# Kernel optimization log

Hardware: AMD Instinct MI355X
Metric: run time of the kernel (lower is better)

Reference implementation:

```python
import jax, jax.numpy as jnp
import numpy as np

B, LQ, LK, D, DV = 8, 2048, 2048, 128, 128


def setup_inputs() -> dict:
    key = jax.random.key(0)
    ks = jax.random.split(key, 6)
    return {
        "query": jax.random.normal(ks[0], (B, LQ, D), dtype=jnp.float32),
        "key": jax.random.normal(ks[1], (B, LK, D), dtype=jnp.float32),
        "value": jax.random.normal(ks[2], (B, LK, DV), dtype=jnp.float32),
        "Wq": jax.random.normal(ks[3], (D, D), dtype=jnp.float32) * 0.08,
        "Wk": jax.random.normal(ks[4], (D, D), dtype=jnp.float32) * 0.08,
        "Wv": jax.random.normal(ks[5], (DV, DV), dtype=jnp.float32) * 0.08,
        "attention_mask": jnp.ones((B, 1, LK), dtype=jnp.int32),
    }


def reference(query, key, value, Wq, Wk, Wv, attention_mask):
    # Linear projections (right-multiplication, as in `x @ W`)
    q = query @ Wq          # [B, lq, n_ed]
    k = key @ Wk            # [B, lk, n_ed]
    v = value @ Wv          # [B, lk, n_ev]
    scale = 1.0 / np.sqrt(q.shape[-1])
    scores = jnp.einsum("bqd,bkd->bqk", q, k) * scale  # [B, lq, lk]
    # additive mask: 0 where attend, -inf where mask==0 (broadcasts)
    mask_vals = jnp.where(attention_mask == 0, -jnp.inf, 0.0).astype(scores.dtype)
    scores = scores + mask_vals
    attn = jax.nn.softmax(scores, axis=-1)
    return attn @ v         # [B, lq, n_ev]
```

## Files before the change

### kernel.cpp

```cpp
#include <hip/hip_runtime.h>
#include <hip/hip_bf16.h>

typedef unsigned short u16;
typedef unsigned int u32;
typedef __attribute__((ext_vector_type(8))) short s8v;
typedef __attribute__((ext_vector_type(4))) float f4v;
typedef __attribute__((ext_vector_type(16))) float f16v;

#define B_N 8
#define L_Q 2048
#define L_K 2048
#define DIM 128
#define KT  64
#define KSPLIT 4
#define KCHUNK (L_K / KSPLIT)

__device__ __forceinline__ u16 f2bf(float f) {
  union { float f; unsigned u; } v; v.f = f;
  return (u16)((v.u + 0x7fffu + ((v.u >> 16) & 1u)) >> 16);
}
__device__ __forceinline__ float bf2f(u16 u) {
  union { u32 u; float f; } v; v.u = ((u32)u) << 16; return v.f;
}
__device__ __forceinline__ u32 packbf2(float a, float b) {
  union { __hip_bfloat162 h; u32 u; } v;
  v.h = __float22bfloat162_rn(make_float2(a, b));
  return v.u;
}
__device__ __forceinline__ void async16(const u16* g, u16* l) {
  __builtin_amdgcn_global_load_lds(
      (const __attribute__((address_space(1))) u32*)(const void*)g,
      (__attribute__((address_space(3))) u32*)(void*)l, 16, 0, 0);
}


__global__ __launch_bounds__(256) void wprep(
    const float* __restrict__ Wq, const float* __restrict__ Wk,
    const float* __restrict__ Wv, u16* __restrict__ wbuf) {
  const int which = blockIdx.x;
  const int tid = threadIdx.x;
  const float* W = (which == 0) ? Wq : (which == 1) ? Wk : Wv;
  const float wscale = (which == 0) ? (1.44269504089f / 11.3137084990f) : 1.0f;
  u16* dst = wbuf + which * 16384;
#pragma unroll
  for (int i = 0; i < 16; ++i) {
    int f4i = tid + i * 256;
    float4 w4 = *(const float4*)(W + f4i * 4);
    int k = f4i >> 5, col = (f4i & 31) * 4;
    int ks = k >> 5, qd = (k & 31) >> 3, j = k & 7;
    float wv4[4] = {w4.x, w4.y, w4.z, w4.w};
#pragma unroll
    for (int c = 0; c < 4; ++c) {
      int n = col + c;
      dst[(ks * 8 + (n >> 4)) * 512 + (qd * 16 + (n & 15)) * 8 + j] = f2bf(wv4[c] * wscale);
    }
  }
}

__global__ __launch_bounds__(256) void proj_mfma(
    const float* __restrict__ query, const float* __restrict__ key,
    const float* __restrict__ value, const u16* __restrict__ wbuf,
    u16* __restrict__ qp, u16* __restrict__ kp, u16* __restrict__ vp) {
  __shared__ __align__(16) u16 Fb[8192];
  const int tid = threadIdx.x;
  const int bi = blockIdx.x;
  const int which = bi >> 8;
  const int sub = bi & 255;
  const int b = sub >> 5;
  const int rt = sub & 31;
  const float* X = (which == 0) ? query : (which == 1) ? key : value;
  const u16* Wfg = wbuf + which * 16384;

  const int w = tid >> 6, lane = tid & 63;
  const int ln = lane & 15, quad = lane >> 4;
  const int xrow = rt * 64 + w * 16 + ln;
  const float* Xr = X + ((size_t)b * L_Q + xrow) * DIM;

  s8v a[4];
#pragma unroll
  for (int ks = 0; ks < 4; ++ks) {
    float4 xa = *(const float4*)(Xr + ks * 32 + quad * 8);
    float4 xb = *(const float4*)(Xr + ks * 32 + quad * 8 + 4);
    s8v t;
    t[0] = (short)f2bf(xa.x); t[1] = (short)f2bf(xa.y);
    t[2] = (short)f2bf(xa.z); t[3] = (short)f2bf(xa.w);
    t[4] = (short)f2bf(xb.x); t[5] = (short)f2bf(xb.y);
    t[6] = (short)f2bf(xb.z); t[7] = (short)f2bf(xb.w);
    a[ks] = t;
  }

  f4v acc[8];
#pragma unroll
  for (int i = 0; i < 8; ++i) acc[i] = (f4v){0.f, 0.f, 0.f, 0.f};
#pragma unroll
  for (int ks = 0; ks < 4; ++ks)
#pragma unroll
    for (int nt = 0; nt < 8; ++nt) {
      s8v bw = *(const s8v*)(Wfg + (ks * 8 + nt) * 512 + lane * 8);
      acc[nt] = __builtin_amdgcn_mfma_f32_16x16x32_bf16(a[ks], bw, acc[nt], 0, 0, 0);
    }

  if (which < 2) {
#pragma unroll
    for (int nt = 0; nt < 8; ++nt) {
      int base = ((w >> 1) * 8 + nt) * 512 + ((ln >> 3) * 32 + (w & 1) * 16 + quad * 4) * 8 + (ln & 7);
#pragma unroll
      for (int r = 0; r < 4; ++r) Fb[base + r * 8] = f2bf(acc[nt][r]);
    }
  } else {
#pragma unroll
    for (int nt = 0; nt < 8; ++nt) {
      int base = (w * 4 + (nt >> 1)) * 512 + ((quad >> 1) * 32 + (nt & 1) * 16 + ln) * 8 + (quad & 1) * 4;
      *(u32*)&Fb[base]     = packbf2(acc[nt][0], acc[nt][1]);
      *(u32*)&Fb[base + 2] = packbf2(acc[nt][2], acc[nt][3]);
    }
  }
  __syncthreads();

  u16* Y = ((which == 0) ? qp : (which == 1) ? kp : vp) + (size_t)(b * 32 + rt) * 8192;
#pragma unroll
  for (int r = 0; r < 4; ++r) {
    int c = tid + r * 256;
    *(s8v*)(Y + c * 8) = *(const s8v*)(Fb + c * 8);
  }
}

__global__ __launch_bounds__(128, 2) void flash_split(
    const u16* __restrict__ qp, const u16* __restrict__ kp,
    const u16* __restrict__ vp, const int* __restrict__ mask,
    u16* __restrict__ po, float* __restrict__ ml) {
  __shared__ __align__(16) u16 Kf[8192];
  __shared__ __align__(16) u16 Vf[8192];
  __shared__ float alphaL[2][32];
  __shared__ float biasl[KT];

  const int tid = threadIdx.x;
  const int bi = blockIdx.x;
  const int b = bi & 7;
  const int rest = bi >> 3;
  const int p = rest & 3;
  const int qb = rest >> 2;
  const int w2 = tid >> 6;
  const int lane = tid & 63;
  const int qcol = lane & 31;
  const int H = lane >> 5;
  const bool Hb = (H != 0);

  const int* mb = mask + b * L_K;

  const u16* Qt = qp + (size_t)(b * 64 + qb * 2 + w2) * 4096;
  s8v aq[8];
#pragma unroll
  for (int c = 0; c < 8; ++c) aq[c] = *(const s8v*)(Qt + c * 512 + lane * 8);

  f16v o[4];
#pragma unroll
  for (int i = 0; i < 4; ++i)
#pragma unroll
    for (int r = 0; r < 16; ++r) o[i][r] = 0.f;
  float mrow = -__builtin_inff();
  float lrow = 0.f;

  for (int it = 0; it < KCHUNK / KT; ++it) {
    const int kt = p * (KCHUNK / KT) + it;
    const int k0 = kt * KT;
    const u16* Ktile = kp + (size_t)(b * 32 + kt) * 8192;
    const u16* Vtile = vp + (size_t)(b * 32 + kt) * 8192;
#pragma unroll
    for (int c8 = 0; c8 < 8; ++c8) {
      int f = w2 * 8 + c8;
      async16(Ktile + (size_t)(f * 64 + lane) * 8, Kf + f * 512);
      async16(Vtile + (size_t)(f * 64 + lane) * 8, Vf + f * 512);
    }
    int mv = mb[k0 + lane];
    bool allones = (__ballot(mv != 0) == ~0ull);
    if (!allones && tid < KT) biasl[tid] = (mv == 0) ? -__builtin_inff() : 0.f;
    __syncthreads();

    f16v s[2];
#pragma unroll
    for (int t = 0; t < 2; ++t)
#pragma unroll
      for (int r = 0; r < 16; ++r) s[t][r] = 0.f;
#pragma unroll
    for (int c = 0; c < 8; ++c) {
      s8v k0f = *(const s8v*)(Kf + c * 512 + lane * 8);
      s[0] = __builtin_amdgcn_mfma_f32_32x32x16_bf16(k0f, aq[c], s[0], 0, 0, 0);
      s8v k1f = *(const s8v*)(Kf + (8 + c) * 512 + lane * 8);
      s[1] = __builtin_amdgcn_mfma_f32_32x32x16_bf16(k1f, aq[c], s[1], 0, 0, 0);
    }
    if (!allones) {
#pragma unroll
      for (int t = 0; t < 2; ++t)
#pragma unroll
        for (int g = 0; g < 4; ++g) {
          float4 bt = *(const float4*)&biasl[t * 32 + g * 8 + 4 * H];
#pragma unroll
          for (int i = 0; i < 4; ++i) s[t][g * 4 + i] += bt.x * (i == 0) + bt.y * (i == 1) + bt.z * (i == 2) + bt.w * (i == 3);
        }
    }
    float m16 = s[0][0];
#pragma unroll
    for (int t = 0; t < 2; ++t)
#pragma unroll
      for (int r = 0; r < 16; ++r) m16 = fmaxf(m16, s[t][r]);
    m16 = fmaxf(m16, __shfl_xor(m16, 32, 64));

    float mn = fmaxf(mrow, m16);
    float alpha = __builtin_amdgcn_exp2f(fminf(mrow - mn, 0.f));
    mrow = mn;
    float rs = 0.f;
#pragma unroll
    for (int t = 0; t < 2; ++t)
#pragma unroll
      for (int r = 0; r < 16; ++r) {
        s[t][r] = __builtin_amdgcn_exp2f(fminf(s[t][r] - mn, 0.f));
        rs += s[t][r];
      }
    rs += __shfl_xor(rs, 32, 64);
    lrow = lrow * alpha + rs;

    if (H == 0) alphaL[w2][qcol] = alpha;

    u32 plo[2][4], phi[2][4];
#pragma unroll
    for (int t = 0; t < 2; ++t)
#pragma unroll
      for (int g = 0; g < 4; ++g) {
        plo[t][g] = packbf2(s[t][g * 4 + 0], s[t][g * 4 + 1]);
        phi[t][g] = packbf2(s[t][g * 4 + 2], s[t][g * 4 + 3]);
      }

#pragma unroll
    for (int g = 0; g < 4; ++g) {
      float4 av = *(const float4*)&alphaL[w2][g * 8 + 4 * H];
      float a4[4] = {av.x, av.y, av.z, av.w};
#pragma unroll
      for (int ntv = 0; ntv < 4; ++ntv)
#pragma unroll
        for (int i = 0; i < 4; ++i) o[ntv][g * 4 + i] *= a4[i];
    }

#pragma unroll
    for (int kc = 0; kc < 4; ++kc) {
      const int t = kc >> 1, gl = (kc & 1) * 2;
      u32 a_lo0 = plo[t][gl], a_hi0 = phi[t][gl];
      u32 a_lo1 = plo[t][gl + 1], a_hi1 = phi[t][gl + 1];
      u32 snd_lo = Hb ? a_lo0 : a_lo1;
      u32 snd_hi = Hb ? a_hi0 : a_hi1;
      u32 r_lo = (u32)__shfl_xor((int)snd_lo, 32, 64);
      u32 r_hi = (u32)__shfl_xor((int)snd_hi, 32, 64);
      union { u32 wd[4]; s8v v; } pa;
      pa.wd[0] = Hb ? r_lo : a_lo0;
      pa.wd[1] = Hb ? r_hi : a_hi0;
      pa.wd[2] = Hb ? a_lo1 : r_lo;
      pa.wd[3] = Hb ? a_hi1 : r_hi;
#pragma unroll
      for (int ntv = 0; ntv < 4; ++ntv) {
        s8v bv = *(const s8v*)(Vf + (kc * 4 + ntv) * 512 + lane * 8);
        o[ntv] = __builtin_amdgcn_mfma_f32_32x32x16_bf16(pa.v, bv, o[ntv], 0, 0, 0);
      }
    }
    __syncthreads();
  }

#pragma unroll
  for (int ntv = 0; ntv < 4; ++ntv)
#pragma unroll
    for (int reg = 0; reg < 16; ++reg) {
      int qloc = (reg & 3) + 8 * (reg >> 2) + 4 * H;
      size_t q = (size_t)b * L_Q + qb * 64 + w2 * 32 + qloc;
      po[(q * KSPLIT + p) * DIM + ntv * 32 + qcol] = f2bf(o[ntv][reg]);
    }
  if (H == 0) {
    size_t q = (size_t)b * L_Q + qb * 64 + w2 * 32 + qcol;
    *(float2*)&ml[(q * KSPLIT + p) * 2] = make_float2(mrow, lrow);
  }
}

__global__ __launch_bounds__(256) void combine(
    const u16* __restrict__ po, const float* __restrict__ ml,
    float* __restrict__ out) {
  const int t = threadIdx.x;
  const int lr = t >> 5, l32 = t & 31;
  const size_t q = (size_t)blockIdx.x * 8 + lr;

  float m[KSPLIT], l[KSPLIT];
#pragma unroll
  for (int p = 0; p < KSPLIT; ++p) {
    m[p] = ml[(q * KSPLIT + p) * 2 + 0];
    l[p] = ml[(q * KSPLIT + p) * 2 + 1];
  }
  float M = m[0];
#pragma unroll
  for (int p = 1; p < KSPLIT; ++p) M = fmaxf(M, m[p]);
  float wp[KSPLIT], L = 0.f;
#pragma unroll
  for (int p = 0; p < KSPLIT; ++p) {
    wp[p] = __builtin_amdgcn_exp2f(fminf(m[p] - M, 0.f));
    L += l[p] * wp[p];
  }
  float invL = 1.0f / L;

  float4 acc = make_float4(0.f, 0.f, 0.f, 0.f);
#pragma unroll
  for (int p = 0; p < KSPLIT; ++p) {
    ushort4 u = *(const ushort4*)(po + (q * KSPLIT + p) * DIM + l32 * 4);
    acc.x += wp[p] * bf2f(u.x); acc.y += wp[p] * bf2f(u.y);
    acc.z += wp[p] * bf2f(u.z); acc.w += wp[p] * bf2f(u.w);
  }
  acc.x *= invL; acc.y *= invL; acc.z *= invL; acc.w *= invL;
  *(float4*)(out + q * DIM + l32 * 4) = acc;
}

extern "C" void kernel_launch(void* const* d_in, const int* in_sizes, int n_in,
                              void* d_out, int out_size, void* d_ws, size_t ws_size,
                              hipStream_t stream) {
  const float* query = (const float*)d_in[0];
  const float* key   = (const float*)d_in[1];
  const float* value = (const float*)d_in[2];
  const float* Wq    = (const float*)d_in[3];
  const float* Wk    = (const float*)d_in[4];
  const float* Wv    = (const float*)d_in[5];
  const int*   mask  = (const int*)d_in[6];
  float* out = (float*)d_out;

  u16* qp = (u16*)d_ws;
  u16* kp = qp + (size_t)B_N * L_Q * DIM;
  u16* vp = kp + (size_t)B_N * L_K * DIM;
  u16* po = vp + (size_t)B_N * DIM * L_K;
  float* ml = (float*)(po + (size_t)B_N * L_Q * KSPLIT * DIM);
  u16* wbuf = (u16*)(ml + (size_t)B_N * L_Q * KSPLIT * 2);

  hipLaunchKernelGGL(wprep, dim3(3), dim3(256), 0, stream, Wq, Wk, Wv, wbuf);
  hipLaunchKernelGGL(proj_mfma, dim3(768), dim3(256), 0, stream,
                     query, key, value, wbuf, qp, kp, vp);
  hipLaunchKernelGGL(flash_split, dim3(1024), dim3(128), 0, stream,
                     qp, kp, vp, mask, po, ml);
  hipLaunchKernelGGL(combine, dim3((B_N * L_Q) / 8), dim3(256), 0, stream,
                     po, ml, out);
}
```

Measured before the change: 126.7 us.

## Double-buffer K/V tiles in flash kernel, widen blocks, stage weights in LDS

After: 122.6 us. 1.03x faster.

```diff
diff --git a/kernel.cpp b/kernel.cpp
--- a/kernel.cpp
+++ b/kernel.cpp
@@ -14,6 +14,7 @@
 #define KT  64
 #define KSPLIT 4
 #define KCHUNK (L_K / KSPLIT)
+#define NIT (KCHUNK / KT)
 
 __device__ __forceinline__ u16 f2bf(float f) {
   union { float f; unsigned u; } v; v.f = f;
@@ -57,10 +58,11 @@
   }
 }
 
-__global__ __launch_bounds__(256) void proj_mfma(
+__global__ __launch_bounds__(256, 3) void proj_mfma(
     const float* __restrict__ query, const float* __restrict__ key,
     const float* __restrict__ value, const u16* __restrict__ wbuf,
     u16* __restrict__ qp, u16* __restrict__ kp, u16* __restrict__ vp) {
+  __shared__ __align__(16) u16 Wf[16384];
   __shared__ __align__(16) u16 Fb[8192];
   const int tid = threadIdx.x;
   const int bi = blockIdx.x;
@@ -73,6 +75,13 @@
 
   const int w = tid >> 6, lane = tid & 63;
   const int ln = lane & 15, quad = lane >> 4;
+
+#pragma unroll
+  for (int c = 0; c < 8; ++c) {
+    int cg = w * 8 + c;
+    async16(Wfg + (size_t)(cg * 64 + lane) * 8, Wf + cg * 512);
+  }
+
   const int xrow = rt * 64 + w * 16 + ln;
   const float* Xr = X + ((size_t)b * L_Q + xrow) * DIM;
 
@@ -81,13 +90,14 @@
   for (int ks = 0; ks < 4; ++ks) {
     float4 xa = *(const float4*)(Xr + ks * 32 + quad * 8);
     float4 xb = *(const float4*)(Xr + ks * 32 + quad * 8 + 4);
-    s8v t;
-    t[0] = (short)f2bf(xa.x); t[1] = (short)f2bf(xa.y);
-    t[2] = (short)f2bf(xa.z); t[3] = (short)f2bf(xa.w);
-    t[4] = (short)f2bf(xb.x); t[5] = (short)f2bf(xb.y);
-    t[6] = (short)f2bf(xb.z); t[7] = (short)f2bf(xb.w);
-    a[ks] = t;
-  }
+    union { u32 wd[4]; s8v v; } t;
+    t.wd[0] = packbf2(xa.x, xa.y);
+    t.wd[1] = packbf2(xa.z, xa.w);
+    t.wd[2] = packbf2(xb.x, xb.y);
+    t.wd[3] = packbf2(xb.z, xb.w);
+    a[ks] = t.v;
+  }
+  __syncthreads();
 
   f4v acc[8];
 #pragma unroll
@@ -96,7 +106,7 @@
   for (int ks = 0; ks < 4; ++ks)
 #pragma unroll
     for (int nt = 0; nt < 8; ++nt) {
-      s8v bw = *(const s8v*)(Wfg + (ks * 8 + nt) * 512 + lane * 8);
+      s8v bw = *(const s8v*)(Wf + (ks * 8 + nt) * 512 + lane * 8);
       acc[nt] = __builtin_amdgcn_mfma_f32_16x16x32_bf16(a[ks], bw, acc[nt], 0, 0, 0);
     }
 
@@ -125,14 +135,14 @@
   }
 }
 
-__global__ __launch_bounds__(128, 2) void flash_split(
+__global__ __launch_bounds__(256, 2) void flash_split(
     const u16* __restrict__ qp, const u16* __restrict__ kp,
     const u16* __restrict__ vp, const int* __restrict__ mask,
     u16* __restrict__ po, float* __restrict__ ml) {
-  __shared__ __align__(16) u16 Kf[8192];
-  __shared__ __align__(16) u16 Vf[8192];
-  __shared__ float alphaL[2][32];
-  __shared__ float biasl[KT];
+  __shared__ __align__(16) u16 Kf[2][8192];
+  __shared__ __align__(16) u16 Vf[2][8192];
+  __shared__ float alphaL[4][32];
+  __shared__ float biasl[2][KT];
 
   const int tid = threadIdx.x;
   const int bi = blockIdx.x;
@@ -140,15 +150,27 @@
   const int rest = bi >> 3;
   const int p = rest & 3;
   const int qb = rest >> 2;
-  const int w2 = tid >> 6;
+  const int w4 = tid >> 6;
   const int lane = tid & 63;
   const int qcol = lane & 31;
   const int H = lane >> 5;
   const bool Hb = (H != 0);
 
   const int* mb = mask + b * L_K;
-
-  const u16* Qt = qp + (size_t)(b * 64 + qb * 2 + w2) * 4096;
+  const int kt0 = p * NIT;
+
+  auto stage = [&](int bufi, int kt_) {
+    const u16* Ktile = kp + (size_t)(b * 32 + kt_) * 8192;
+    const u16* Vtile = vp + (size_t)(b * 32 + kt_) * 8192;
+#pragma unroll
+    for (int c = 0; c < 4; ++c) {
+      int f = w4 * 4 + c;
+      async16(Ktile + (size_t)(f * 64 + lane) * 8, &Kf[bufi][f * 512]);
+      async16(Vtile + (size_t)(f * 64 + lane) * 8, &Vf[bufi][f * 512]);
+    }
+  };
+
+  const u16* Qt = qp + (size_t)(b * 64 + qb * 4 + w4) * 4096;
   s8v aq[8];
 #pragma unroll
   for (int c = 0; c < 8; ++c) aq[c] = *(const s8v*)(Qt + c * 512 + lane * 8);
@@ -161,21 +183,22 @@
   float mrow = -__builtin_inff();
   float lrow = 0.f;
 
-  for (int it = 0; it < KCHUNK / KT; ++it) {
-    const int kt = p * (KCHUNK / KT) + it;
-    const int k0 = kt * KT;
-    const u16* Ktile = kp + (size_t)(b * 32 + kt) * 8192;
-    const u16* Vtile = vp + (size_t)(b * 32 + kt) * 8192;
-#pragma unroll
-    for (int c8 = 0; c8 < 8; ++c8) {
-      int f = w2 * 8 + c8;
-      async16(Ktile + (size_t)(f * 64 + lane) * 8, Kf + f * 512);
-      async16(Vtile + (size_t)(f * 64 + lane) * 8, Vf + f * 512);
-    }
-    int mv = mb[k0 + lane];
-    bool allones = (__ballot(mv != 0) == ~0ull);
-    if (!allones && tid < KT) biasl[tid] = (mv == 0) ? -__builtin_inff() : 0.f;
-    __syncthreads();
+  stage(0, kt0);
+  int mv0 = mb[kt0 * KT + lane];
+  bool ao_next = (__ballot(mv0 != 0) == ~0ull);
+  if (!ao_next && tid < KT) biasl[0][tid] = (mv0 == 0) ? -__builtin_inff() : 0.f;
+  __syncthreads();
+
+  for (int it = 0; it < NIT; ++it) {
+    const int cur = it & 1;
+    const bool allones = ao_next;
+
+    if (it + 1 < NIT) {
+      stage(cur ^ 1, kt0 + it + 1);
+      int mv = mb[(kt0 + it + 1) * KT + lane];
+      ao_next = (__ballot(mv != 0) == ~0ull);
+      if (!ao_next && tid < KT) biasl[cur ^ 1][tid] = (mv == 0) ? -__builtin_inff() : 0.f;
+    }
 
     f16v s[2];
 #pragma unroll
@@ -184,9 +207,9 @@
       for (int r = 0; r < 16; ++r) s[t][r] = 0.f;
 #pragma unroll
     for (int c = 0; c < 8; ++c) {
-      s8v k0f = *(const s8v*)(Kf + c * 512 + lane * 8);
+      s8v k0f = *(const s8v*)(&Kf[cur][c * 512] + lane * 8);
       s[0] = __builtin_amdgcn_mfma_f32_32x32x16_bf16(k0f, aq[c], s[0], 0, 0, 0);
-      s8v k1f = *(const s8v*)(Kf + (8 + c) * 512 + lane * 8);
+      s8v k1f = *(const s8v*)(&Kf[cur][(8 + c) * 512] + lane * 8);
       s[1] = __builtin_amdgcn_mfma_f32_32x32x16_bf16(k1f, aq[c], s[1], 0, 0, 0);
     }
     if (!allones) {
@@ -194,9 +217,9 @@
       for (int t = 0; t < 2; ++t)
 #pragma unroll
         for (int g = 0; g < 4; ++g) {
-          float4 bt = *(const float4*)&biasl[t * 32 + g * 8 + 4 * H];
-#pragma unroll
-          for (int i = 0; i < 4; ++i) s[t][g * 4 + i] += bt.x * (i == 0) + bt.y * (i == 1) + bt.z * (i == 2) + bt.w * (i == 3);
+          float4 bt = *(const float4*)&biasl[cur][t * 32 + g * 8 + 4 * H];
+          s[t][g * 4 + 0] += bt.x; s[t][g * 4 + 1] += bt.y;
+          s[t][g * 4 + 2] += bt.z; s[t][g * 4 + 3] += bt.w;
         }
     }
     float m16 = s[0][0];
@@ -220,7 +243,7 @@
     rs += __shfl_xor(rs, 32, 64);
     lrow = lrow * alpha + rs;
 
-    if (H == 0) alphaL[w2][qcol] = alpha;
+    if (H == 0) alphaL[w4][qcol] = alpha;
 
     u32 plo[2][4], phi[2][4];
 #pragma unroll
@@ -233,7 +256,7 @@
 
 #pragma unroll
     for (int g = 0; g < 4; ++g) {
-      float4 av = *(const float4*)&alphaL[w2][g * 8 + 4 * H];
+      float4 av = *(const float4*)&alphaL[w4][g * 8 + 4 * H];
       float a4[4] = {av.x, av.y, av.z, av.w};
 #pragma unroll
       for (int ntv = 0; ntv < 4; ++ntv)
@@ -257,7 +280,7 @@
       pa.wd[3] = Hb ? a_hi1 : r_hi;
 #pragma unroll
       for (int ntv = 0; ntv < 4; ++ntv) {
-        s8v bv = *(const s8v*)(Vf + (kc * 4 + ntv) * 512 + lane * 8);
+        s8v bv = *(const s8v*)(&Vf[cur][(kc * 4 + ntv) * 512] + lane * 8);
         o[ntv] = __builtin_amdgcn_mfma_f32_32x32x16_bf16(pa.v, bv, o[ntv], 0, 0, 0);
       }
     }
@@ -269,11 +292,11 @@
 #pragma unroll
     for (int reg = 0; reg < 16; ++reg) {
       int qloc = (reg & 3) + 8 * (reg >> 2) + 4 * H;
-      size_t q = (size_t)b * L_Q + qb * 64 + w2 * 32 + qloc;
+      size_t q = (size_t)b * L_Q + qb * 128 + w4 * 32 + qloc;
       po[(q * KSPLIT + p) * DIM + ntv * 32 + qcol] = f2bf(o[ntv][reg]);
     }
   if (H == 0) {
-    size_t q = (size_t)b * L_Q + qb * 64 + w2 * 32 + qcol;
+    size_t q = (size_t)b * L_Q + qb * 128 + w4 * 32 + qcol;
     *(float2*)&ml[(q * KSPLIT + p) * 2] = make_float2(mrow, lrow);
   }
 }
@@ -335,7 +358,7 @@
   hipLaunchKernelGGL(wprep, dim3(3), dim3(256), 0, stream, Wq, Wk, Wv, wbuf);
   hipLaunchKernelGGL(proj_mfma, dim3(768), dim3(256), 0, stream,
                      query, key, value, wbuf, qp, kp, vp);
-  hipLaunchKernelGGL(flash_split, dim3(1024), dim3(128), 0, stream,
+  hipLaunchKernelGGL(flash_split, dim3(512), dim3(256), 0, stream,
                      qp, kp, vp, mask, po, ml);
   hipLaunchKernelGGL(combine, dim3((B_N * L_Q) / 8), dim3(256), 0, stream,
                      po, ml, out);
```
